# Kernel tuning notes

Measured on AMD Instinct MI355X. Metric: run time of the kernel, lower is better.

The kernel has to match this reference:

```python
import jax, jax.numpy as jnp
import numpy as np

B, L, E, H = 2, 2048, 1024, 16
HD = E // H


def _rel_shift(x):
    # x: [b, h, q, k] -> Transformer-XL relative shift via pad+reshape trick
    b, h, q, k = x.shape
    xp = jnp.pad(x, ((0, 0), (0, 0), (0, 0), (1, 0)))  # pad left of last dim
    xp = xp.reshape(b, h, k + 1, q)
    return xp[:, :, 1:, :].reshape(b, h, q, k)


def setup_inputs() -> dict:
    key = jax.random.key(0)
    ks = jax.random.split(key, 16)
    s = 0.02
    return {
        "query": jax.random.normal(ks[0], (B, L, E), jnp.float32),
        "key": jax.random.normal(ks[1], (B, L, E), jnp.float32),
        "value": jax.random.normal(ks[2], (B, L, E), jnp.float32),
        "pos_embedding": jax.random.normal(ks[3], (B, L, E), jnp.float32),
        "Wq": jax.random.normal(ks[4], (E, E), jnp.float32) * s,
        "bq": jnp.zeros((E,), jnp.float32),
        "Wk": jax.random.normal(ks[5], (E, E), jnp.float32) * s,
        "bk": jnp.zeros((E,), jnp.float32),
        "Wv": jax.random.normal(ks[6], (E, E), jnp.float32) * s,
        "bv": jnp.zeros((E,), jnp.float32),
        "Wp": jax.random.normal(ks[7], (E, E), jnp.float32) * s,  # Pos linear, no bias
        "Wo": jax.random.normal(ks[8], (E, E), jnp.float32) * s,
        "bo": jnp.zeros((E,), jnp.float32),
        "U": jax.random.normal(ks[9], (H, HD), jnp.float32) * s,
        "V": jax.random.normal(ks[10], (H, HD), jnp.float32) * s,
    }


def reference(query, key, value, pos_embedding, Wq, bq, Wk, bk, Wv, bv, Wp, Wo, bo, U, V):
    b, qlen, e = query.shape
    h, hd = U.shape
    scale = jnp.sqrt(jnp.asarray(e, query.dtype))
    # torch Linear: y = x @ W.T + b
    q = (query @ Wq.T + bq).reshape(b, qlen, h, hd)
    k = (key @ Wk.T + bk).reshape(b, key.shape[1], h, hd)
    v = (value @ Wv.T + bv).reshape(b, value.shape[1], h, hd)
    r = (pos_embedding @ Wp.T).reshape(b, -1, h, hd)
    content_score = jnp.einsum("bqhd,bkhd->bhqk", q + U, k)
    position_score = jnp.einsum("bqhd,bkhd->bhqk", q + V, r)
    position_score = _rel_shift(position_score)
    attention_score = (content_score + position_score) / scale
    # NOTE: the original module applies NO softmax; faithful reproduction.
    # einsum 'bhqk,bvhd->bqhd' sums over both k (scores) and v (values).
    alpha = jnp.einsum("bhqk,bvhd->bqhd", attention_score, v).reshape(b, qlen, e)
    return alpha @ Wo.T + bo
```

## Files before the change

### kernel.cpp

```cpp
#include <hip/hip_runtime.h>

#define BB 2
#define LL 2048
#define EE 1024
#define HH 16
#define HDD 64

typedef __bf16 bf16x8 __attribute__((ext_vector_type(8)));
typedef float f32x4 __attribute__((ext_vector_type(4)));

__device__ __forceinline__ unsigned short f2bf(float f) {
  unsigned int x = __float_as_uint(f);
  return (unsigned short)((x + 0x7FFFu + ((x >> 16) & 1u)) >> 16);
}

__device__ __forceinline__ float bf2f(unsigned short u) {
  return __uint_as_float((unsigned int)u << 16);
}

__device__ __forceinline__ void load_lds16(const void* g, void* l) {
  __builtin_amdgcn_global_load_lds(
      (const __attribute__((address_space(1))) void*)g,
      (__attribute__((address_space(3))) void*)l, 16, 0, 0);
}

#define SUMKV_BLOCKS 256
#define CAST_BLOCKS 1280
#define CAST_STRIDE (CAST_BLOCKS * 256)
__global__ __launch_bounds__(256) void prelude_kernel(
    const float* __restrict__ q, const float* __restrict__ pe,
    const float* __restrict__ wq, const float* __restrict__ wp,
    unsigned short* __restrict__ q16, unsigned short* __restrict__ pe16,
    unsigned short* __restrict__ wq16, unsigned short* __restrict__ wp16,
    const float* __restrict__ key, const float* __restrict__ value,
    float* __restrict__ keysum, float* __restrict__ valsum) {
  if (blockIdx.x < SUMKV_BLOCKS) {
    int blk2 = blockIdx.x;
    int b = blk2 >> 7, ch = blk2 & 127;
    int tid = threadIdx.x;
    const float4* k4 = (const float4*)(key   + ((size_t)b * LL + ch * 16) * EE);
    const float4* v4 = (const float4*)(value + ((size_t)b * LL + ch * 16) * EE);
    float4 ak = make_float4(0.f, 0.f, 0.f, 0.f);
    float4 av = make_float4(0.f, 0.f, 0.f, 0.f);
#pragma unroll 8
    for (int i = 0; i < 16; i++) {
      float4 kk = k4[i * 256 + tid];
      float4 vv = v4[i * 256 + tid];
      ak.x += kk.x; ak.y += kk.y; ak.z += kk.z; ak.w += kk.w;
      av.x += vv.x; av.y += vv.y; av.z += vv.z; av.w += vv.w;
    }
    int e = tid * 4;
    atomicAdd(&keysum[b * EE + e + 0], ak.x);
    atomicAdd(&keysum[b * EE + e + 1], ak.y);
    atomicAdd(&keysum[b * EE + e + 2], ak.z);
    atomicAdd(&keysum[b * EE + e + 3], ak.w);
    atomicAdd(&valsum[b * EE + e + 0], av.x);
    atomicAdd(&valsum[b * EE + e + 1], av.y);
    atomicAdd(&valsum[b * EE + e + 2], av.z);
    atomicAdd(&valsum[b * EE + e + 3], av.w);
  } else {
    const int NQ4 = BB * LL * EE / 4;
    const int NW4 = EE * EE / 4;
    int t = (blockIdx.x - SUMKV_BLOCKS) * 256 + threadIdx.x;
    float4 v[8]; unsigned short* dst[8]; int off[8];
#pragma unroll
    for (int k = 0; k < 8; k++) {
      int i = t + k * CAST_STRIDE;
      const float* src;
      if (i < NQ4)                { src = q;  dst[k] = q16;  off[k] = i; }
      else if (i < 2 * NQ4)       { src = pe; dst[k] = pe16; off[k] = i - NQ4; }
      else if (i < 2 * NQ4 + NW4) { src = wq; dst[k] = wq16; off[k] = i - 2 * NQ4; }
      else                        { src = wp; dst[k] = wp16; off[k] = i - 2 * NQ4 - NW4; }
      v[k] = ((const float4*)src)[off[k]];
    }
#pragma unroll
    for (int k = 0; k < 8; k++) {
      ushort4 u;
      u.x = f2bf(v[k].x); u.y = f2bf(v[k].y); u.z = f2bf(v[k].z); u.w = f2bf(v[k].w);
      ((ushort4*)dst[k])[off[k]] = u;
    }
  }
}

__global__ __launch_bounds__(256) void proj_kernel(
    const float* __restrict__ keysum, const float* __restrict__ valsum,
    const float* __restrict__ Wk, const float* __restrict__ bk,
    const float* __restrict__ Wv, const float* __restrict__ bv,
    float* __restrict__ Kproj, float* __restrict__ Vproj) {
  int wv = threadIdx.x >> 6, lane = threadIdx.x & 63;
  int idx = blockIdx.x * 4 + wv;
  int b = idx >> 10, ep = idx & (EE - 1);
  const float* sum  = blockIdx.z ? valsum : keysum;
  const float* W    = blockIdx.z ? Wv : Wk;
  const float* bias = blockIdx.z ? bv : bk;
  float* outp       = blockIdx.z ? Vproj : Kproj;
  float acc = 0.f;
  for (int k = lane; k < EE; k += 64) acc += sum[b * EE + k] * W[ep * EE + k];
  for (int off = 32; off; off >>= 1) acc += __shfl_down(acc, off, 64);
  if (lane == 0) outp[b * EE + ep] = acc + (float)LL * bias[ep];
}

__global__ __launch_bounds__(256) void w2_kernel(
    const float* __restrict__ Vproj, const float* __restrict__ Wo,
    float* __restrict__ W2) {
  int wv = threadIdx.x >> 6, lane = threadIdx.x & 63;
  int idx = blockIdx.x * 4 + wv;
  int e = idx & (EE - 1);
  int h = (idx >> 10) & (HH - 1);
  int b = idx >> 14;
  float acc = Vproj[b * EE + h * HDD + lane] * Wo[(size_t)e * EE + h * HDD + lane];
  for (int off = 32; off; off >>= 1) acc += __shfl_down(acc, off, 64);
  if (lane == 0) W2[((size_t)b * HH + h) * EE + e] = acc;
}

__global__ __launch_bounds__(256) void gemm_kernel(
    const unsigned short* __restrict__ q16, const unsigned short* __restrict__ wq16,
    const float* __restrict__ bq, unsigned short* __restrict__ qout,
    const unsigned short* __restrict__ pe16, const unsigned short* __restrict__ wp16,
    unsigned short* __restrict__ rout, float* __restrict__ chunks) {
  const int K = EE, N = EE;
  const unsigned short* X; const unsigned short* W; const float* bias;
  unsigned short* Out;
  if (blockIdx.z == 0) { X = q16;  W = wq16; bias = bq;      Out = qout; }
  else                 { X = pe16; W = wp16; bias = nullptr; Out = rout; }

  __shared__ __align__(16) unsigned short As[128 * 32];
  __shared__ __align__(16) unsigned short Bs[128 * 32];

  const int tid = threadIdx.x;
  const int lane = tid & 63;
  const int wv = tid >> 6;
  const int wr = wv >> 1, wc = wv & 1;
  const int n0 = blockIdx.x * 128;
  const int m0 = blockIdx.y * 128;

  const int srow = wv * 16 + (lane >> 2);
  const int scol = (lane & 3) * 8;
  const unsigned short* gA = X + (size_t)(m0 + srow) * K + scol;
  const unsigned short* gB = W + (size_t)(n0 + srow) * K + scol;
  unsigned short* sA = As + wv * 512;
  unsigned short* sB = Bs + wv * 512;

  f32x4 acc[4][4];
#pragma unroll
  for (int i = 0; i < 4; i++)
#pragma unroll
    for (int j = 0; j < 4; j++) acc[i][j] = (f32x4)0.0f;

  const int arow = wr * 64 + (lane & 15);
  const int brow = wc * 64 + (lane & 15);
  const int koff = (lane >> 4) * 8;

  for (int kk = 0; kk < K; kk += 32) {
    load_lds16(gA + kk,                   sA);
    load_lds16(gA + kk + (size_t)64 * K,  sA + 2048);
    load_lds16(gB + kk,                   sB);
    load_lds16(gB + kk + (size_t)64 * K,  sB + 2048);
    __syncthreads();
    bf16x8 af[4], bf[4];
#pragma unroll
    for (int i = 0; i < 4; i++) af[i] = *(const bf16x8*)&As[(arow + i * 16) * 32 + koff];
#pragma unroll
    for (int j = 0; j < 4; j++) bf[j] = *(const bf16x8*)&Bs[(brow + j * 16) * 32 + koff];
#pragma unroll
    for (int i = 0; i < 4; i++)
#pragma unroll
      for (int j = 0; j < 4; j++)
        acc[i][j] = __builtin_amdgcn_mfma_f32_16x16x32_bf16(af[i], bf[j], acc[i][j], 0, 0, 0);
    __syncthreads();
  }

  const int rbase = m0 + wr * 64 + (lane >> 4) * 4;
  const int cbase = n0 + wc * 64 + (lane & 15);
#pragma unroll
  for (int i = 0; i < 4; i++) {
#pragma unroll
    for (int j = 0; j < 4; j++) {
      int col = cbase + j * 16;
      float badd = bias ? bias[col] : 0.f;
#pragma unroll
      for (int g = 0; g < 4; g++) {
        int row = rbase + i * 16 + g;
        Out[(size_t)row * N + col] = f2bf(acc[i][j][g] + badd);
      }
    }
  }

  if (blockIdx.z == 1) {
    int b = m0 >> 11;
    int ch0 = ((m0 & (LL - 1)) >> 5) + wr * 2;
#pragma unroll
    for (int cp = 0; cp < 2; cp++) {
#pragma unroll
      for (int j = 0; j < 4; j++) {
        float s = 0.f;
#pragma unroll
        for (int i = cp * 2; i < cp * 2 + 2; i++)
#pragma unroll
          for (int g = 0; g < 4; g++) s += acc[i][j][g];
        s += __shfl_down(s, 32, 64);
        s += __shfl_down(s, 16, 64);
        if (lane < 16) {
          int col = n0 + wc * 64 + j * 16 + lane;
          chunks[((size_t)b * 64 + ch0 + cp) * EE + col] = s;
        }
      }
    }
  }
}

__global__ __launch_bounds__(256) void scan2f_kernel(
    const unsigned short* __restrict__ qbuf, const unsigned short* __restrict__ rbuf,
    const float* __restrict__ chunks, const float* __restrict__ Kproj,
    const float* __restrict__ U, const float* __restrict__ V,
    float* __restrict__ S1, float* __restrict__ Dbuf) {
  int tid = threadIdx.x, lane = tid & 63;
  int hg = blockIdx.x, ch = blockIdx.y, b = blockIdx.z;
  int e = hg * 256 + tid;
  int h = hg * 4 + (tid >> 6);
  float pre = 0.f, tot = 0.f;
  for (int c = 0; c < 64; c++) {
    float cs = chunks[((size_t)b * 64 + c) * EE + e];
    tot += cs;
    if (c < ch) pre += cs;
  }
  float kp = Kproj[b * EE + e], Ue = U[e], Ve = V[e];
  float run = pre;
  size_t hoff = ((size_t)b * HH + h) * LL;
#pragma unroll 4
  for (int i = 0; i < 32; i++) {
    int m = ch * 32 + i;
    int p = LL - 1 - m;
    float qv = bf2f(qbuf[((size_t)b * LL + p) * EE + e]);
    float rv = bf2f(rbuf[((size_t)b * LL + m) * EE + e]);
    float tq = qv + Ve;
    float d = tq * run;
    float s = tq * tot + (qv + Ue) * kp;
#pragma unroll
    for (int off = 32; off; off >>= 1) {
      d += __shfl_down(d, off, 64);
      s += __shfl_down(s, off, 64);
    }
    if (lane == 0) { Dbuf[hoff + m] = d; S1[hoff + p] = s; }
    run += rv;
  }
}

__global__ __launch_bounds__(256) void out_kernel(
    const float* __restrict__ S1, const float* __restrict__ Dbuf,
    const float* __restrict__ W2, const float* __restrict__ bo,
    float* __restrict__ out) {
  int row = blockIdx.x;
  int b = row >> 11, p = row & (LL - 1);
  __shared__ float sh[HH];
  if (threadIdx.x < HH) {
    int h = threadIdx.x;
    size_t hoff = ((size_t)b * HH + h) * LL;
    float s1 = S1[hoff + p];
    float d1 = Dbuf[hoff + (LL - 1 - p)];
    float d2 = (p == LL - 1) ? 0.f : Dbuf[hoff + (LL - 2 - p)];
    sh[h] = (s1 - d1 + d2) * (1.f / 32.f);
  }
  __syncthreads();
  int e4 = threadIdx.x;
  const float4* W2v = (const float4*)W2;
  float4 acc = ((const float4*)bo)[e4];
#pragma unroll
  for (int h = 0; h < HH; h++) {
    float s = sh[h];
    float4 w = W2v[((size_t)b * HH + h) * 256 + e4];
    acc.x += s * w.x; acc.y += s * w.y; acc.z += s * w.z; acc.w += s * w.w;
  }
  ((float4*)out)[(size_t)row * 256 + e4] = acc;
}

extern "C" void kernel_launch(void* const* d_in, const int* in_sizes, int n_in,
                              void* d_out, int out_size, void* d_ws, size_t ws_size,
                              hipStream_t stream) {
  const float* query = (const float*)d_in[0];
  const float* key   = (const float*)d_in[1];
  const float* value = (const float*)d_in[2];
  const float* pos   = (const float*)d_in[3];
  const float* Wq = (const float*)d_in[4];
  const float* bq = (const float*)d_in[5];
  const float* Wk = (const float*)d_in[6];
  const float* bk = (const float*)d_in[7];
  const float* Wv = (const float*)d_in[8];
  const float* bv = (const float*)d_in[9];
  const float* Wp = (const float*)d_in[10];
  const float* Wo = (const float*)d_in[11];
  const float* bo = (const float*)d_in[12];
  const float* U  = (const float*)d_in[13];
  const float* V  = (const float*)d_in[14];
  float* out = (float*)d_out;

  char* ws = (char*)d_ws;
  size_t o = 0;
  auto take = [&](size_t bytes) -> char* {
    char* p = ws + o;
    o += (bytes + 255) & ~(size_t)255;
    return p;
  };
  float* keysum = (float*)take(BB * EE * 4);
  float* valsum = (float*)take(BB * EE * 4);
  float* Kproj  = (float*)take(BB * EE * 4);
  float* Vproj  = (float*)take(BB * EE * 4);
  float* W2     = (float*)take((size_t)BB * HH * EE * 4);
  float* S1     = (float*)take((size_t)BB * HH * LL * 4);
  float* Dbuf   = (float*)take((size_t)BB * HH * LL * 4);
  float* chunks = (float*)take((size_t)BB * 64 * EE * 4);
  unsigned short* qbuf = (unsigned short*)take((size_t)BB * LL * EE * 2);
  unsigned short* rbuf = (unsigned short*)take((size_t)BB * LL * EE * 2);
  unsigned short* q16  = (unsigned short*)take((size_t)BB * LL * EE * 2);
  unsigned short* pe16 = (unsigned short*)take((size_t)BB * LL * EE * 2);
  unsigned short* wq16 = (unsigned short*)take((size_t)EE * EE * 2);
  unsigned short* wp16 = (unsigned short*)take((size_t)EE * EE * 2);

  hipMemsetAsync(keysum, 0, (size_t)2 * BB * EE * 4, stream);

  prelude_kernel<<<SUMKV_BLOCKS + CAST_BLOCKS, 256, 0, stream>>>(
      query, pos, Wq, Wp, q16, pe16, wq16, wp16, key, value, keysum, valsum);
  proj_kernel<<<dim3(BB * EE / 4, 1, 2), 256, 0, stream>>>(
      keysum, valsum, Wk, bk, Wv, bv, Kproj, Vproj);
  w2_kernel<<<dim3(BB * HH * EE / 4), 256, 0, stream>>>(Vproj, Wo, W2);
  gemm_kernel<<<dim3(EE / 128, BB * LL / 128, 2), 256, 0, stream>>>(
      q16, wq16, bq, qbuf, pe16, wp16, rbuf, chunks);
  scan2f_kernel<<<dim3(4, 64, BB), 256, 0, stream>>>(qbuf, rbuf, chunks, Kproj, U, V, S1, Dbuf);
  out_kernel<<<dim3(BB * LL), 256, 0, stream>>>(S1, Dbuf, W2, bo, out);
}
```

Baseline: 234.3 us.

## Fuse W2 computation into GEMM launch, swap grid axes, batch out_kernel rows

Removes the separate w2_kernel launch by making the W2 (Vproj·Wo per head) work an extra z-slice of the GEMM grid, so it runs alongside the projection GEMMs. Each wave now computes 32 output columns instead of one, reusing its Vproj value. The GEMM grid axes are swapped so blockIdx.x walks M instead of N, which changes the tile scheduling order. out_kernel now processes 8 rows per block and holds W2 in registers, so W2 is read once per block instead of once per row, at the cost of more registers per thread.

```diff
diff --git a/kernel.cpp b/kernel.cpp
--- a/kernel.cpp
+++ b/kernel.cpp
@@ -100,24 +100,34 @@
   if (lane == 0) outp[b * EE + ep] = acc + (float)LL * bias[ep];
 }
 
-__global__ __launch_bounds__(256) void w2_kernel(
-    const float* __restrict__ Vproj, const float* __restrict__ Wo,
-    float* __restrict__ W2) {
-  int wv = threadIdx.x >> 6, lane = threadIdx.x & 63;
-  int idx = blockIdx.x * 4 + wv;
-  int e = idx & (EE - 1);
-  int h = (idx >> 10) & (HH - 1);
-  int b = idx >> 14;
-  float acc = Vproj[b * EE + h * HDD + lane] * Wo[(size_t)e * EE + h * HDD + lane];
-  for (int off = 32; off; off >>= 1) acc += __shfl_down(acc, off, 64);
-  if (lane == 0) W2[((size_t)b * HH + h) * EE + e] = acc;
-}
-
 __global__ __launch_bounds__(256) void gemm_kernel(
     const unsigned short* __restrict__ q16, const unsigned short* __restrict__ wq16,
     const float* __restrict__ bq, unsigned short* __restrict__ qout,
     const unsigned short* __restrict__ pe16, const unsigned short* __restrict__ wp16,
-    unsigned short* __restrict__ rout, float* __restrict__ chunks) {
+    unsigned short* __restrict__ rout, float* __restrict__ chunks,
+    const float* __restrict__ Vproj, const float* __restrict__ Wo,
+    float* __restrict__ W2) {
+  const int tid = threadIdx.x;
+  const int lane = tid & 63;
+  const int wv = tid >> 6;
+
+  if (blockIdx.z == 2) {
+    int bid = blockIdx.x + 32 * blockIdx.y;
+    int wslot = bid * 4 + wv;
+    int base = wslot * 32;
+    int b = base >> 14;
+    int h = (base >> 10) & (HH - 1);
+    int e0 = base & (EE - 1);
+    float vp = Vproj[b * EE + h * HDD + lane];
+    const float* wo = Wo + (size_t)e0 * EE + h * HDD + lane;
+    for (int r = 0; r < 32; r++) {
+      float acc = vp * wo[(size_t)r * EE];
+      for (int off = 32; off; off >>= 1) acc += __shfl_down(acc, off, 64);
+      if (lane == 0) W2[((size_t)b * HH + h) * EE + e0 + r] = acc;
+    }
+    return;
+  }
+
   const int K = EE, N = EE;
   const unsigned short* X; const unsigned short* W; const float* bias;
   unsigned short* Out;
@@ -127,12 +137,9 @@
   __shared__ __align__(16) unsigned short As[128 * 32];
   __shared__ __align__(16) unsigned short Bs[128 * 32];
 
-  const int tid = threadIdx.x;
-  const int lane = tid & 63;
-  const int wv = tid >> 6;
   const int wr = wv >> 1, wc = wv & 1;
-  const int n0 = blockIdx.x * 128;
-  const int m0 = blockIdx.y * 128;
+  const int m0 = blockIdx.x * 128;
+  const int n0 = blockIdx.y * 128;
 
   const int srow = wv * 16 + (lane >> 2);
   const int scol = (lane & 3) * 8;
@@ -250,28 +257,36 @@
     const float* __restrict__ S1, const float* __restrict__ Dbuf,
     const float* __restrict__ W2, const float* __restrict__ bo,
     float* __restrict__ out) {
-  int row = blockIdx.x;
-  int b = row >> 11, p = row & (LL - 1);
-  __shared__ float sh[HH];
-  if (threadIdx.x < HH) {
-    int h = threadIdx.x;
+  int row0 = blockIdx.x * 8;
+  int b = row0 >> 11, p0 = row0 & (LL - 1);
+  int tid = threadIdx.x;
+  __shared__ float sh[8][HH];
+  if (tid < 128) {
+    int rr = tid >> 4, h = tid & 15;
+    int p = p0 + rr;
     size_t hoff = ((size_t)b * HH + h) * LL;
     float s1 = S1[hoff + p];
     float d1 = Dbuf[hoff + (LL - 1 - p)];
     float d2 = (p == LL - 1) ? 0.f : Dbuf[hoff + (LL - 2 - p)];
-    sh[h] = (s1 - d1 + d2) * (1.f / 32.f);
-  }
+    sh[rr][h] = (s1 - d1 + d2) * (1.f / 32.f);
+  }
+  float4 w2r[HH];
+#pragma unroll
+  for (int h = 0; h < HH; h++)
+    w2r[h] = ((const float4*)(W2 + ((size_t)b * HH + h) * EE))[tid];
+  float4 bo4 = ((const float4*)bo)[tid];
   __syncthreads();
-  int e4 = threadIdx.x;
-  const float4* W2v = (const float4*)W2;
-  float4 acc = ((const float4*)bo)[e4];
-#pragma unroll
-  for (int h = 0; h < HH; h++) {
-    float s = sh[h];
-    float4 w = W2v[((size_t)b * HH + h) * 256 + e4];
-    acc.x += s * w.x; acc.y += s * w.y; acc.z += s * w.z; acc.w += s * w.w;
-  }
-  ((float4*)out)[(size_t)row * 256 + e4] = acc;
+#pragma unroll
+  for (int rr = 0; rr < 8; rr++) {
+    float4 acc = bo4;
+#pragma unroll
+    for (int h = 0; h < HH; h++) {
+      float s = sh[rr][h];
+      acc.x += s * w2r[h].x; acc.y += s * w2r[h].y;
+      acc.z += s * w2r[h].z; acc.w += s * w2r[h].w;
+    }
+    ((float4*)out)[(size_t)(row0 + rr) * 256 + tid] = acc;
+  }
 }
 
 extern "C" void kernel_launch(void* const* d_in, const int* in_sizes, int n_in,
@@ -322,9 +337,8 @@
       query, pos, Wq, Wp, q16, pe16, wq16, wp16, key, value, keysum, valsum);
   proj_kernel<<<dim3(BB * EE / 4, 1, 2), 256, 0, stream>>>(
       keysum, valsum, Wk, bk, Wv, bv, Kproj, Vproj);
-  w2_kernel<<<dim3(BB * HH * EE / 4), 256, 0, stream>>>(Vproj, Wo, W2);
-  gemm_kernel<<<dim3(EE / 128, BB * LL / 128, 2), 256, 0, stream>>>(
-      q16, wq16, bq, qbuf, pe16, wp16, rbuf, chunks);
+  gemm_kernel<<<dim3(BB * LL / 128, EE / 128, 3), 256, 0, stream>>>(
+      q16, wq16, bq, qbuf, pe16, wp16, rbuf, chunks, Vproj, Wo, W2);
   scan2f_kernel<<<dim3(4, 64, BB), 256, 0, stream>>>(qbuf, rbuf, chunks, Kproj, U, V, S1, Dbuf);
-  out_kernel<<<dim3(BB * LL), 256, 0, stream>>>(S1, Dbuf, W2, bo, out);
-}
+  out_kernel<<<dim3(BB * LL / 8), 256, 0, stream>>>(S1, Dbuf, W2, bo, out);
+}
```

New measurement: 222.8 us. 1.05x faster.
